# Kernel tuning notes

Hardware: AMD Instinct MI355X
Metric: run time of the kernel (lower is better)

## Reference

```python
import jax, jax.numpy as jnp
import numpy as np

B, S, D_MODEL, H = 2, 2048, 1024, 16
DEPTH = D_MODEL // H


def setup_inputs() -> dict:
    key = jax.random.key(0)
    ks = jax.random.split(key, 12)
    s = 1.0 / np.sqrt(D_MODEL)
    inp = {
        "q": jax.random.normal(ks[0], (B, S, D_MODEL), jnp.float32),
        "k": jax.random.normal(ks[1], (B, S, D_MODEL), jnp.float32),
        "v": jax.random.normal(ks[2], (B, S, D_MODEL), jnp.float32),
        # CTRL-style causal mask: 1 where position is disallowed (future), 0 otherwise
        "mask": jnp.triu(jnp.ones((S, S), jnp.float32), k=1),
        "Wq_w": jax.random.normal(ks[3], (D_MODEL, D_MODEL), jnp.float32) * s,
        "Wq_b": jax.random.normal(ks[4], (D_MODEL,), jnp.float32) * s,
        "Wk_w": jax.random.normal(ks[5], (D_MODEL, D_MODEL), jnp.float32) * s,
        "Wk_b": jax.random.normal(ks[6], (D_MODEL,), jnp.float32) * s,
        "Wv_w": jax.random.normal(ks[7], (D_MODEL, D_MODEL), jnp.float32) * s,
        "Wv_b": jax.random.normal(ks[8], (D_MODEL,), jnp.float32) * s,
        "dense_w": jax.random.normal(ks[9], (D_MODEL, D_MODEL), jnp.float32) * s,
        "dense_b": jax.random.normal(ks[10], (D_MODEL,), jnp.float32) * s,
    }
    return inp


def _split_heads(x):
    # [B, S, D] -> [B, H, S, depth]
    b, s, _ = x.shape
    return x.reshape(b, s, H, DEPTH).transpose(0, 2, 1, 3)


def reference(q, k, v, mask, Wq_w, Wq_b, Wk_w, Wk_b, Wv_w, Wv_b, dense_w, dense_b):
    b = q.shape[0]
    # torch Linear: y = x @ W^T + b
    qh = _split_heads(q @ Wq_w.T + Wq_b)  # [B,H,Sq,dh]
    kh = _split_heads(k @ Wk_w.T + Wk_b)  # [B,H,Sk,dh]
    vh = _split_heads(v @ Wv_w.T + Wv_b)  # [B,H,Sk,dh]

    scale = 1.0 / np.sqrt(DEPTH)
    logits = jnp.einsum("bhqd,bhkd->bhqk", qh, kh) * scale  # [B,H,Sq,Sk]
    nd, ns = logits.shape[-2], logits.shape[-1]
    logits = logits + mask[ns - nd:ns, :ns] * -10000.0
    attn = jax.nn.softmax(logits, axis=-1)
    ctx = jnp.einsum("bhqk,bhkd->bhqd", attn, vh)  # [B,H,Sq,dh]
    ctx = ctx.transpose(0, 2, 1, 3).reshape(b, -1, D_MODEL)  # [B,Sq,D]
    out = ctx @ dense_w.T + dense_b
    return out
```

## Files before the change

### kernel.cpp

```cpp
#include <hip/hip_runtime.h>
#include <hip/hip_bf16.h>

typedef __bf16 bf16x8 __attribute__((ext_vector_type(8)));
typedef __bf16 bf16x4 __attribute__((ext_vector_type(4)));
typedef float  f32x4  __attribute__((ext_vector_type(4)));

#define D_MODEL 1024
#define SEQ     2048
#define NH      16
#define DH      64
#define MTOT    4096

__device__ __forceinline__ void gload16(const void* gp, void* lp) {
  __builtin_amdgcn_global_load_lds(
      (const __attribute__((address_space(1))) unsigned int*)gp,
      (__attribute__((address_space(3))) unsigned int*)lp,
      16, 0, 0);
}

struct CvtSegs {
  const float* s[7];
  __bf16*      d[7];
  int          n8[7];
};

__global__ __launch_bounds__(256) void cvt_kernel(CvtSegs c) {
  const int seg = blockIdx.y;
  const float4* s = (const float4*)c.s[seg];
  bf16x8*       d = (bf16x8*)c.d[seg];
  const int n8 = c.n8[seg];
  for (int i = blockIdx.x * 256 + threadIdx.x; i < n8; i += gridDim.x * 256) {
    float4 a = s[2 * i];
    float4 b = s[2 * i + 1];
    bf16x8 o;
    o[0] = (__bf16)a.x; o[1] = (__bf16)a.y; o[2] = (__bf16)a.z; o[3] = (__bf16)a.w;
    o[4] = (__bf16)b.x; o[5] = (__bf16)b.y; o[6] = (__bf16)b.z; o[7] = (__bf16)b.w;
    d[i] = o;
  }
}

template <int EPI>
__device__ __forceinline__ void gemm_core(const __bf16* __restrict__ A,
                                          const __bf16* __restrict__ W,
                                          const float* __restrict__ bias,
                                          void* __restrict__ outp,
                                          __bf16* Asm, __bf16* Bsm,
                                          int row0, int col0) {
  const int tid = threadIdx.x;
  const int lane = tid & 63;
  const int w = tid >> 6;
  const int lr = lane & 15, lg = lane >> 4;
  const int wr = w >> 1, wc = w & 1;
  char* AsB = (char*)Asm;
  char* BsB = (char*)Bsm;

  f32x4 acc[4][4];
#pragma unroll
  for (int i = 0; i < 4; ++i)
#pragma unroll
    for (int j = 0; j < 4; ++j) acc[i][j] = (f32x4){0.f, 0.f, 0.f, 0.f};

  const int kch = (lane & 3) * 8;

#pragma unroll
  for (int tt = 0; tt < 2; ++tt) {
#pragma unroll
    for (int s = 0; s < 2; ++s) {
      const int cb = (w * 2 + s) * 64;
      const int arow = (cb + lane) >> 2;
      gload16(A + (size_t)(row0 + arow) * D_MODEL + tt * 32 + kch,
              AsB + tt * 8192 + cb * 16);
      gload16(W + (size_t)(col0 + arow) * D_MODEL + tt * 32 + kch,
              BsB + tt * 8192 + cb * 16);
    }
  }

  for (int t = 0; t < 32; ++t) {
    if (t < 31) asm volatile("s_waitcnt vmcnt(4)" ::: "memory");
    else        asm volatile("s_waitcnt vmcnt(0)" ::: "memory");
    __builtin_amdgcn_s_barrier();
    if (t + 2 < 32) {
      const int nb = (t + 2) % 3;
      const int k0 = (t + 2) * 32;
#pragma unroll
      for (int s = 0; s < 2; ++s) {
        const int cb = (w * 2 + s) * 64;
        const int arow = (cb + lane) >> 2;
        gload16(A + (size_t)(row0 + arow) * D_MODEL + k0 + kch,
                AsB + nb * 8192 + cb * 16);
        gload16(W + (size_t)(col0 + arow) * D_MODEL + k0 + kch,
                BsB + nb * 8192 + cb * 16);
      }
    }
    {
      char* Ab = AsB + (t % 3) * 8192;
      char* Bb = BsB + (t % 3) * 8192;
      bf16x8 af[4], bfr[4];
#pragma unroll
      for (int mi = 0; mi < 4; ++mi)
        af[mi] = *(const bf16x8*)(Ab + (wr * 64 + mi * 16 + lr) * 64 + lg * 16);
#pragma unroll
      for (int ni = 0; ni < 4; ++ni)
        bfr[ni] = *(const bf16x8*)(Bb + (wc * 64 + ni * 16 + lr) * 64 + lg * 16);
      __builtin_amdgcn_s_setprio(1);
#pragma unroll
      for (int mi = 0; mi < 4; ++mi)
#pragma unroll
        for (int ni = 0; ni < 4; ++ni)
          acc[mi][ni] = __builtin_amdgcn_mfma_f32_16x16x32_bf16(af[mi], bfr[ni],
                                                                acc[mi][ni], 0, 0, 0);
      __builtin_amdgcn_s_setprio(0);
      __builtin_amdgcn_sched_barrier(0);
    }
  }

  if (EPI == 2) {
    __bf16* o = (__bf16*)outp;
#pragma unroll
    for (int mi = 0; mi < 4; ++mi) {
#pragma unroll
      for (int ni = 0; ni < 4; ++ni) {
        const int n = col0 + wc * 64 + ni * 16 + lr;
        const float bv = bias[n];
        const int m0 = row0 + wr * 64 + mi * 16 + lg * 4;
        bf16x4 pk;
#pragma unroll
        for (int j = 0; j < 4; ++j) pk[j] = (__bf16)(acc[mi][ni][j] + bv);
        *(bf16x4*)(o + ((size_t)((m0 >> 11) * NH + (n >> 6)) * DH + (n & 63)) * SEQ +
                   (m0 & 2047)) = pk;
      }
    }
  } else {
#pragma unroll
    for (int mi = 0; mi < 4; ++mi) {
#pragma unroll
      for (int ni = 0; ni < 4; ++ni) {
        const int n = col0 + wc * 64 + ni * 16 + lr;
        const float bv = bias[n];
#pragma unroll
        for (int j = 0; j < 4; ++j) {
          const int m = row0 + wr * 64 + mi * 16 + lg * 4 + j;
          const float v = acc[mi][ni][j] + bv;
          if (EPI == 0) {
            __bf16* o = (__bf16*)outp;
            o[(size_t)((m >> 11) * NH + (n >> 6)) * (SEQ * DH) +
              (size_t)(m & 2047) * DH + (n & 63)] = (__bf16)v;
          } else {
            float* o = (float*)outp;
            o[(size_t)m * D_MODEL + n] = v;
          }
        }
      }
    }
  }
}

struct QkvPtrs {
  const __bf16* A[3];
  const __bf16* W[3];
  const float*  b[3];
  __bf16*       o[3];
};

__global__ __launch_bounds__(256, 3) void gemm_qkv_kernel(QkvPtrs p) {
  __shared__ __bf16 As[3][128 * 32];
  __shared__ __bf16 Bs[3][128 * 32];
  const int z = blockIdx.z;
  if (z == 2)
    gemm_core<2>(p.A[z], p.W[z], p.b[z], p.o[z], &As[0][0], &Bs[0][0],
                 blockIdx.x * 128, blockIdx.y * 128);
  else
    gemm_core<0>(p.A[z], p.W[z], p.b[z], p.o[z], &As[0][0], &Bs[0][0],
                 blockIdx.x * 128, blockIdx.y * 128);
}

__global__ __launch_bounds__(256, 3) void gemm_out_kernel(const __bf16* __restrict__ A,
                                                          const __bf16* __restrict__ W,
                                                          const float* __restrict__ b,
                                                          float* __restrict__ o) {
  __shared__ __bf16 As[3][128 * 32];
  __shared__ __bf16 Bs[3][128 * 32];
  gemm_core<1>(A, W, b, o, &As[0][0], &Bs[0][0], blockIdx.x * 128, blockIdx.y * 128);
}

__global__ __launch_bounds__(256, 2) void attn_kernel(const __bf16* __restrict__ qh,
                                                      const __bf16* __restrict__ kh,
                                                      const __bf16* __restrict__ vt,
                                                      __bf16* __restrict__ ctx) {
  __shared__ __align__(16) char LDS[81920];

  const int bh = blockIdx.x;
  const int qb = 31 - blockIdx.y;
  const int tid = threadIdx.x, lane = tid & 63, w = tid >> 6;
  const int lr = lane & 15, lg = lane >> 4;
  const size_t hoff = (size_t)bh * SEQ * DH;
  const __bf16* Q   = qh + hoff;
  const __bf16* Kp  = kh + hoff;
  const __bf16* Vtp = vt + hoff;
  const int q0 = qb * 64;

  bf16x8 qf[4][2];
#pragma unroll
  for (int qi = 0; qi < 4; ++qi)
#pragma unroll
    for (int ki = 0; ki < 2; ++ki)
      qf[qi][ki] = *(const bf16x8*)(Q + (size_t)(q0 + qi * 16 + lr) * DH +
                                    ki * 32 + lg * 8);

  f32x4 o[4][4];
#pragma unroll
  for (int qi = 0; qi < 4; ++qi)
#pragma unroll
    for (int ni = 0; ni < 4; ++ni) o[qi][ni] = (f32x4){0.f, 0.f, 0.f, 0.f};
  float ls[4] = {0.f, 0.f, 0.f, 0.f};

  char* Kl = LDS + w * 20480;
  char* Vl = Kl + 8192;
  char* Pl = Kl + 16384;

  const int ntt = 2 * qb + 2;
  const int cnt = (ntt - w + 3) >> 2;

#define STAGE_TILE(T, B)                                                      \
  {                                                                           \
    _Pragma("unroll") for (int g = 0; g < 4; ++g) {                           \
      const int c = g * 64 + lane;                                            \
      const int kr = c >> 3, kc2 = (c & 7) ^ (kr & 7);                        \
      gload16(Kp + (size_t)((T) * 32 + kr) * DH + kc2 * 8,                    \
              Kl + (B) * 4096 + g * 1024);                                    \
    }                                                                         \
    _Pragma("unroll") for (int g = 0; g < 4; ++g) {                           \
      const int c = g * 64 + lane;                                            \
      const int vr = c >> 2, vc2 = (c & 3) ^ (vr & 3);                        \
      gload16(Vtp + (size_t)vr * SEQ + (T) * 32 + vc2 * 8,                    \
              Vl + (B) * 4096 + g * 1024);                                    \
    }                                                                         \
  }

  if (cnt > 0) STAGE_TILE(w, 0);

  int cur = 0;
  for (int it = 0; it < cnt; ++it) {
    const int t = w + it * 4;
    if (it + 1 < cnt) {
      STAGE_TILE(t + 4, cur ^ 1);
      asm volatile("s_waitcnt vmcnt(8)" ::: "memory");
    } else {
      asm volatile("s_waitcnt vmcnt(0)" ::: "memory");
    }
    __builtin_amdgcn_sched_barrier(0);
    char* Kb = Kl + cur * 4096;
    char* Vb = Vl + cur * 4096;

    f32x4 st[2][4];
#pragma unroll
    for (int ni = 0; ni < 2; ++ni)
#pragma unroll
      for (int qi = 0; qi < 4; ++qi) st[ni][qi] = (f32x4){0.f, 0.f, 0.f, 0.f};
    __builtin_amdgcn_s_setprio(1);
#pragma unroll
    for (int ki = 0; ki < 2; ++ki) {
#pragma unroll
      for (int ni = 0; ni < 2; ++ni) {
        const int kr = ni * 16 + lr;
        bf16x8 kf = *(const bf16x8*)(Kb + kr * 128 +
                                     (((ki * 4 + lg) ^ (kr & 7)) << 4));
#pragma unroll
        for (int qi = 0; qi < 4; ++qi)
          st[ni][qi] = __builtin_amdgcn_mfma_f32_16x16x32_bf16(kf, qf[qi][ki],
                                                               st[ni][qi], 0, 0, 0);
      }
    }
    __builtin_amdgcn_s_setprio(0);

    const int kvb = t * 32;
    const bool needmask = (kvb + 31 > q0);
#pragma unroll
    for (int ni = 0; ni < 2; ++ni) {
#pragma unroll
      for (int qi = 0; qi < 4; ++qi) {
        bf16x4 pk;
#pragma unroll
        for (int j = 0; j < 4; ++j) {
          float v = st[ni][qi][j] * 0.18033688f;
          if (needmask && (kvb + ni * 16 + lg * 4 + j > q0 + qi * 16 + lr))
            v = -1e9f;
          const float pe = __builtin_amdgcn_exp2f(v);
          ls[qi] += pe;
          pk[j] = (__bf16)pe;
        }
        const int q = qi * 16 + lr;
        const int ch = (ni * 2 + (lg >> 1)) ^ (q & 3);
        *(bf16x4*)(Pl + q * 64 + ch * 16 + (lg & 1) * 8) = pk;
      }
    }
    asm volatile("s_waitcnt lgkmcnt(0)" ::: "memory");
    __builtin_amdgcn_sched_barrier(0);

    bf16x8 pf[4], vf[4];
#pragma unroll
    for (int qi = 0; qi < 4; ++qi) {
      const int q = qi * 16 + lr;
      pf[qi] = *(const bf16x8*)(Pl + q * 64 + ((lg ^ (q & 3)) << 4));
    }
#pragma unroll
    for (int ni = 0; ni < 4; ++ni) {
      const int d = ni * 16 + lr;
      vf[ni] = *(const bf16x8*)(Vb + d * 64 + ((lg ^ (d & 3)) << 4));
    }
    __builtin_amdgcn_s_setprio(1);
#pragma unroll
    for (int qi = 0; qi < 4; ++qi)
#pragma unroll
      for (int ni = 0; ni < 4; ++ni)
        o[qi][ni] = __builtin_amdgcn_mfma_f32_16x16x32_bf16(pf[qi], vf[ni],
                                                            o[qi][ni], 0, 0, 0);
    __builtin_amdgcn_s_setprio(0);
    cur ^= 1;
  }
#undef STAGE_TILE

  __syncthreads();
  float* Op = (float*)LDS + w * 4352;
#pragma unroll
  for (int qi = 0; qi < 4; ++qi)
#pragma unroll
    for (int ni = 0; ni < 4; ++ni)
      *(f32x4*)(Op + (ni * 16 + lr) * 68 + qi * 16 + lg * 4) = o[qi][ni];
  {
    float* Lp = (float*)LDS + 17408 + (w * 4 + lg) * 64;
#pragma unroll
    for (int qi = 0; qi < 4; ++qi) Lp[qi * 16 + lr] = ls[qi];
  }
  __syncthreads();

  f32x4 a2[4];
#pragma unroll
  for (int r = 0; r < 4; ++r) a2[r] = (f32x4){0.f, 0.f, 0.f, 0.f};
#pragma unroll
  for (int p = 0; p < 4; ++p) {
    const float* Pp = (const float*)LDS + p * 4352;
#pragma unroll
    for (int r = 0; r < 4; ++r)
      a2[r] += *(const f32x4*)(Pp + (r * 16 + lr) * 68 + w * 16 + lg * 4);
  }
  float Lt = 0.f;
#pragma unroll
  for (int k = 0; k < 4; ++k)
    Lt += ((const float*)LDS)[17408 + (k * 4 + lg) * 64 + w * 16 + lr];
  Lt += __shfl_xor(Lt, 16, 64);
  Lt += __shfl_xor(Lt, 32, 64);

  const int bb = bh >> 4, hh = bh & 15;
#pragma unroll
  for (int j = 0; j < 4; ++j) {
    const float inv = 1.0f / __shfl(Lt, lg * 4 + j, 16);
    const int qrow = q0 + w * 16 + lg * 4 + j;
    __bf16* orow = ctx + (size_t)(bb * SEQ + qrow) * D_MODEL + hh * DH;
#pragma unroll
    for (int r = 0; r < 4; ++r)
      orow[r * 16 + lr] = (__bf16)(a2[r][j] * inv);
  }
}

extern "C" void kernel_launch(void* const* d_in, const int* in_sizes, int n_in,
                              void* d_out, int out_size, void* d_ws, size_t ws_size,
                              hipStream_t stream) {
  (void)in_sizes; (void)n_in; (void)out_size; (void)ws_size;
  const float* q  = (const float*)d_in[0];
  const float* k  = (const float*)d_in[1];
  const float* v  = (const float*)d_in[2];
  const float* Wq = (const float*)d_in[4];
  const float* bq = (const float*)d_in[5];
  const float* Wk = (const float*)d_in[6];
  const float* bk = (const float*)d_in[7];
  const float* Wv = (const float*)d_in[8];
  const float* bv = (const float*)d_in[9];
  const float* Wd = (const float*)d_in[10];
  const float* bd = (const float*)d_in[11];

  char* ws = (char*)d_ws;
  __bf16* qb  = (__bf16*)(ws + 0);
  __bf16* kb  = (__bf16*)(ws + 8388608);
  __bf16* vb  = (__bf16*)(ws + 16777216);
  __bf16* wqb = (__bf16*)(ws + 25165824);
  __bf16* wkb = (__bf16*)(ws + 27262976);
  __bf16* wvb = (__bf16*)(ws + 29360128);
  __bf16* wdb = (__bf16*)(ws + 31457280);
  __bf16* qhp = (__bf16*)(ws + 33554432);
  __bf16* khp = (__bf16*)(ws + 41943040);
  __bf16* vtp = (__bf16*)(ws + 50331648);
  __bf16* ctxp= (__bf16*)(ws + 58720256);

  CvtSegs cs;
  cs.s[0] = q;  cs.d[0] = qb;  cs.n8[0] = 524288;
  cs.s[1] = k;  cs.d[1] = kb;  cs.n8[1] = 524288;
  cs.s[2] = v;  cs.d[2] = vb;  cs.n8[2] = 524288;
  cs.s[3] = Wq; cs.d[3] = wqb; cs.n8[3] = 131072;
  cs.s[4] = Wk; cs.d[4] = wkb; cs.n8[4] = 131072;
  cs.s[5] = Wv; cs.d[5] = wvb; cs.n8[5] = 131072;
  cs.s[6] = Wd; cs.d[6] = wdb; cs.n8[6] = 131072;
  cvt_kernel<<<dim3(256, 7, 1), dim3(256), 0, stream>>>(cs);

  QkvPtrs qp;
  qp.A[0] = qb;  qp.A[1] = kb;  qp.A[2] = vb;
  qp.W[0] = wqb; qp.W[1] = wkb; qp.W[2] = wvb;
  qp.b[0] = bq;  qp.b[1] = bk;  qp.b[2] = bv;
  qp.o[0] = qhp; qp.o[1] = khp; qp.o[2] = vtp;
  gemm_qkv_kernel<<<dim3(32, 8, 3), dim3(256), 0, stream>>>(qp);

  attn_kernel<<<dim3(32, 32, 1), dim3(256), 0, stream>>>(qhp, khp, vtp, ctxp);

  gemm_out_kernel<<<dim3(32, 8, 1), dim3(256), 0, stream>>>(ctxp, wdb, bd, (float*)d_out);
}
```

Baseline: 114.9 us.

## Use 256x256 tiles with 512-thread blocks for the QKV projection GEMM

The fused QKV projection moves from 128x128 tiles with 256 threads to 256x256 tiles with 512 threads (8 waves, each computing 128x64), keeping triple-buffered LDS staging via global_load_lds. Larger tiles double the arithmetic done per loaded element and cut global/L2 traffic for the A and W operands. The grid shrinks from 768 to 192 blocks, which can underfill a 256-CU device and leave tail imbalance, and the larger accumulator arrays raise register pressure. The output GEMM is split into its own f32-epilogue core and is otherwise unchanged.

Result: slower. 128.6 us (+11.9%).

```diff
diff --git a/kernel.cpp b/kernel.cpp
--- a/kernel.cpp
+++ b/kernel.cpp
@@ -40,12 +40,131 @@
 }
 
 template <int EPI>
-__device__ __forceinline__ void gemm_core(const __bf16* __restrict__ A,
-                                          const __bf16* __restrict__ W,
-                                          const float* __restrict__ bias,
-                                          void* __restrict__ outp,
-                                          __bf16* Asm, __bf16* Bsm,
-                                          int row0, int col0) {
+__device__ __forceinline__ void gemm256_core(const __bf16* __restrict__ A,
+                                             const __bf16* __restrict__ W,
+                                             const float* __restrict__ bias,
+                                             void* __restrict__ outp,
+                                             __bf16* Asm, __bf16* Bsm,
+                                             int row0, int col0) {
+  const int tid = threadIdx.x;
+  const int lane = tid & 63;
+  const int w = tid >> 6;
+  const int lr = lane & 15, lg = lane >> 4;
+  const int wr = w >> 2, wc = w & 3;
+  char* AsB = (char*)Asm;
+  char* BsB = (char*)Bsm;
+
+  f32x4 acc[8][4];
+#pragma unroll
+  for (int i = 0; i < 8; ++i)
+#pragma unroll
+    for (int j = 0; j < 4; ++j) acc[i][j] = (f32x4){0.f, 0.f, 0.f, 0.f};
+
+#define STAGE256(TT, B)                                                       \
+  {                                                                           \
+    _Pragma("unroll") for (int s = 0; s < 2; ++s) {                           \
+      const int cb = (s * 8 + w) * 64;                                        \
+      const int c = cb + lane;                                                \
+      const int row = c >> 2;                                                 \
+      const int kch = (c & 3) * 8;                                            \
+      gload16(A + (size_t)(row0 + row) * D_MODEL + (TT) * 32 + kch,           \
+              AsB + (B) * 16384 + cb * 16);                                   \
+      gload16(W + (size_t)(col0 + row) * D_MODEL + (TT) * 32 + kch,           \
+              BsB + (B) * 16384 + cb * 16);                                   \
+    }                                                                         \
+  }
+
+  STAGE256(0, 0);
+  STAGE256(1, 1);
+
+  for (int t = 0; t < 32; ++t) {
+    if (t < 31) asm volatile("s_waitcnt vmcnt(4)" ::: "memory");
+    else        asm volatile("s_waitcnt vmcnt(0)" ::: "memory");
+    __builtin_amdgcn_s_barrier();
+    if (t + 2 < 32) STAGE256(t + 2, (t + 2) % 3);
+    {
+      char* Ab = AsB + (t % 3) * 16384;
+      char* Bb = BsB + (t % 3) * 16384;
+      bf16x8 af[8], bfr[4];
+#pragma unroll
+      for (int mi = 0; mi < 8; ++mi)
+        af[mi] = *(const bf16x8*)(Ab + (wr * 128 + mi * 16 + lr) * 64 + lg * 16);
+#pragma unroll
+      for (int ni = 0; ni < 4; ++ni)
+        bfr[ni] = *(const bf16x8*)(Bb + (wc * 64 + ni * 16 + lr) * 64 + lg * 16);
+      __builtin_amdgcn_s_setprio(1);
+#pragma unroll
+      for (int mi = 0; mi < 8; ++mi)
+#pragma unroll
+        for (int ni = 0; ni < 4; ++ni)
+          acc[mi][ni] = __builtin_amdgcn_mfma_f32_16x16x32_bf16(af[mi], bfr[ni],
+                                                                acc[mi][ni], 0, 0, 0);
+      __builtin_amdgcn_s_setprio(0);
+      __builtin_amdgcn_sched_barrier(0);
+    }
+  }
+#undef STAGE256
+
+  if (EPI == 2) {
+    __bf16* o = (__bf16*)outp;
+#pragma unroll
+    for (int mi = 0; mi < 8; ++mi) {
+#pragma unroll
+      for (int ni = 0; ni < 4; ++ni) {
+        const int n = col0 + wc * 64 + ni * 16 + lr;
+        const float bv = bias[n];
+        const int m0 = row0 + wr * 128 + mi * 16 + lg * 4;
+        bf16x4 pk;
+#pragma unroll
+        for (int j = 0; j < 4; ++j) pk[j] = (__bf16)(acc[mi][ni][j] + bv);
+        *(bf16x4*)(o + ((size_t)((m0 >> 11) * NH + (n >> 6)) * DH + (n & 63)) * SEQ +
+                   (m0 & 2047)) = pk;
+      }
+    }
+  } else {
+#pragma unroll
+    for (int mi = 0; mi < 8; ++mi) {
+#pragma unroll
+      for (int ni = 0; ni < 4; ++ni) {
+        const int n = col0 + wc * 64 + ni * 16 + lr;
+        const float bv = bias[n];
+#pragma unroll
+        for (int j = 0; j < 4; ++j) {
+          const int m = row0 + wr * 128 + mi * 16 + lg * 4 + j;
+          __bf16* o = (__bf16*)outp;
+          o[(size_t)((m >> 11) * NH + (n >> 6)) * (SEQ * DH) +
+            (size_t)(m & 2047) * DH + (n & 63)] = (__bf16)(acc[mi][ni][j] + bv);
+        }
+      }
+    }
+  }
+}
+
+struct QkvPtrs {
+  const __bf16* A[3];
+  const __bf16* W[3];
+  const float*  b[3];
+  __bf16*       o[3];
+};
+
+__global__ __launch_bounds__(512, 2) void gemm_qkv_kernel(QkvPtrs p) {
+  __shared__ __bf16 As[3][256 * 32];
+  __shared__ __bf16 Bs[3][256 * 32];
+  const int z = blockIdx.z;
+  if (z == 2)
+    gemm256_core<2>(p.A[z], p.W[z], p.b[z], p.o[z], &As[0][0], &Bs[0][0],
+                    blockIdx.x * 256, blockIdx.y * 256);
+  else
+    gemm256_core<0>(p.A[z], p.W[z], p.b[z], p.o[z], &As[0][0], &Bs[0][0],
+                    blockIdx.x * 256, blockIdx.y * 256);
+}
+
+__device__ __forceinline__ void gemm_core_f32(const __bf16* __restrict__ A,
+                                              const __bf16* __restrict__ W,
+                                              const float* __restrict__ bias,
+                                              float* __restrict__ outp,
+                                              __bf16* Asm, __bf16* Bsm,
+                                              int row0, int col0) {
   const int tid = threadIdx.x;
   const int lane = tid & 63;
   const int w = tid >> 6;
@@ -114,64 +233,19 @@
     }
   }
 
-  if (EPI == 2) {
-    __bf16* o = (__bf16*)outp;
-#pragma unroll
-    for (int mi = 0; mi < 4; ++mi) {
-#pragma unroll
-      for (int ni = 0; ni < 4; ++ni) {
-        const int n = col0 + wc * 64 + ni * 16 + lr;
-        const float bv = bias[n];
-        const int m0 = row0 + wr * 64 + mi * 16 + lg * 4;
-        bf16x4 pk;
-#pragma unroll
-        for (int j = 0; j < 4; ++j) pk[j] = (__bf16)(acc[mi][ni][j] + bv);
-        *(bf16x4*)(o + ((size_t)((m0 >> 11) * NH + (n >> 6)) * DH + (n & 63)) * SEQ +
-                   (m0 & 2047)) = pk;
-      }
-    }
-  } else {
-#pragma unroll
-    for (int mi = 0; mi < 4; ++mi) {
-#pragma unroll
-      for (int ni = 0; ni < 4; ++ni) {
-        const int n = col0 + wc * 64 + ni * 16 + lr;
-        const float bv = bias[n];
-#pragma unroll
-        for (int j = 0; j < 4; ++j) {
-          const int m = row0 + wr * 64 + mi * 16 + lg * 4 + j;
-          const float v = acc[mi][ni][j] + bv;
-          if (EPI == 0) {
-            __bf16* o = (__bf16*)outp;
-            o[(size_t)((m >> 11) * NH + (n >> 6)) * (SEQ * DH) +
-              (size_t)(m & 2047) * DH + (n & 63)] = (__bf16)v;
-          } else {
-            float* o = (float*)outp;
-            o[(size_t)m * D_MODEL + n] = v;
-          }
-        }
-      }
-    }
-  }
-}
-
-struct QkvPtrs {
-  const __bf16* A[3];
-  const __bf16* W[3];
-  const float*  b[3];
-  __bf16*       o[3];
-};
-
-__global__ __launch_bounds__(256, 3) void gemm_qkv_kernel(QkvPtrs p) {
-  __shared__ __bf16 As[3][128 * 32];
-  __shared__ __bf16 Bs[3][128 * 32];
-  const int z = blockIdx.z;
-  if (z == 2)
-    gemm_core<2>(p.A[z], p.W[z], p.b[z], p.o[z], &As[0][0], &Bs[0][0],
-                 blockIdx.x * 128, blockIdx.y * 128);
-  else
-    gemm_core<0>(p.A[z], p.W[z], p.b[z], p.o[z], &As[0][0], &Bs[0][0],
-                 blockIdx.x * 128, blockIdx.y * 128);
+#pragma unroll
+  for (int mi = 0; mi < 4; ++mi) {
+#pragma unroll
+    for (int ni = 0; ni < 4; ++ni) {
+      const int n = col0 + wc * 64 + ni * 16 + lr;
+      const float bv = bias[n];
+#pragma unroll
+      for (int j = 0; j < 4; ++j) {
+        const int m = row0 + wr * 64 + mi * 16 + lg * 4 + j;
+        outp[(size_t)m * D_MODEL + n] = acc[mi][ni][j] + bv;
+      }
+    }
+  }
 }
 
 __global__ __launch_bounds__(256, 3) void gemm_out_kernel(const __bf16* __restrict__ A,
@@ -180,7 +254,7 @@
                                                           float* __restrict__ o) {
   __shared__ __bf16 As[3][128 * 32];
   __shared__ __bf16 Bs[3][128 * 32];
-  gemm_core<1>(A, W, b, o, &As[0][0], &Bs[0][0], blockIdx.x * 128, blockIdx.y * 128);
+  gemm_core_f32(A, W, b, o, &As[0][0], &Bs[0][0], blockIdx.x * 128, blockIdx.y * 128);
 }
 
 __global__ __launch_bounds__(256, 2) void attn_kernel(const __bf16* __restrict__ qh,
@@ -407,7 +481,7 @@
   qp.W[0] = wqb; qp.W[1] = wkb; qp.W[2] = wvb;
   qp.b[0] = bq;  qp.b[1] = bk;  qp.b[2] = bv;
   qp.o[0] = qhp; qp.o[1] = khp; qp.o[2] = vtp;
-  gemm_qkv_kernel<<<dim3(32, 8, 3), dim3(256), 0, stream>>>(qp);
+  gemm_qkv_kernel<<<dim3(16, 4, 3), dim3(512), 0, stream>>>(qp);
 
   attn_kernel<<<dim3(32, 32, 1), dim3(256), 0, stream>>>(qhp, khp, vtp, ctxp);
 
```

## Shrink attention KV tile to 16 and keep P in registers via k16 MFMA

Applied to the files above, without the earlier changes.

The attention kernel now processes 16-key tiles per wave instead of 32, so the exponentiated scores stay in registers and feed a 16x16x16 bf16 MFMA directly as the B operand, with no round trip through LDS for P. LDS per block drops by half, so launch bounds move from 2 to 3 blocks per CU for higher occupancy. The cross-wave reduction now stores partial outputs as bf16 in a transposed layout. In exchange the loop runs twice as many iterations with smaller MFMAs, and the bf16 partial sums lose some precision.

Result: faster. 112.6 us (-2.0%).

```diff
diff --git a/kernel.cpp b/kernel.cpp
--- a/kernel.cpp
+++ b/kernel.cpp
@@ -4,12 +4,21 @@
 typedef __bf16 bf16x8 __attribute__((ext_vector_type(8)));
 typedef __bf16 bf16x4 __attribute__((ext_vector_type(4)));
 typedef float  f32x4  __attribute__((ext_vector_type(4)));
+typedef short  s16x4  __attribute__((ext_vector_type(4)));
 
 #define D_MODEL 1024
 #define SEQ     2048
 #define NH      16
 #define DH      64
 #define MTOT    4096
+
+__device__ __forceinline__ f32x4 mfma_bf16_k16(s16x4 a, s16x4 b, f32x4 c) {
+#if defined(__HIP_DEVICE_COMPILE__)
+  return __builtin_amdgcn_mfma_f32_16x16x16bf16_1k(a, b, c, 0, 0, 0);
+#else
+  return c;
+#endif
+}
 
 __device__ __forceinline__ void gload16(const void* gp, void* lp) {
   __builtin_amdgcn_global_load_lds(
@@ -183,11 +192,11 @@
   gemm_core<1>(A, W, b, o, &As[0][0], &Bs[0][0], blockIdx.x * 128, blockIdx.y * 128);
 }
 
-__global__ __launch_bounds__(256, 2) void attn_kernel(const __bf16* __restrict__ qh,
+__global__ __launch_bounds__(256, 3) void attn_kernel(const __bf16* __restrict__ qh,
                                                       const __bf16* __restrict__ kh,
                                                       const __bf16* __restrict__ vt,
                                                       __bf16* __restrict__ ctx) {
-  __shared__ __align__(16) char LDS[81920];
+  __shared__ __align__(16) char LDS[40960];
 
   const int bh = blockIdx.x;
   const int qb = 31 - blockIdx.y;
@@ -207,128 +216,115 @@
       qf[qi][ki] = *(const bf16x8*)(Q + (size_t)(q0 + qi * 16 + lr) * DH +
                                     ki * 32 + lg * 8);
 
-  f32x4 o[4][4];
-#pragma unroll
-  for (int qi = 0; qi < 4; ++qi)
-#pragma unroll
-    for (int ni = 0; ni < 4; ++ni) o[qi][ni] = (f32x4){0.f, 0.f, 0.f, 0.f};
+  f32x4 o2[4][4];
+#pragma unroll
+  for (int ni = 0; ni < 4; ++ni)
+#pragma unroll
+    for (int qi = 0; qi < 4; ++qi) o2[ni][qi] = (f32x4){0.f, 0.f, 0.f, 0.f};
   float ls[4] = {0.f, 0.f, 0.f, 0.f};
 
-  char* Kl = LDS + w * 20480;
-  char* Vl = Kl + 8192;
-  char* Pl = Kl + 16384;
-
-  const int ntt = 2 * qb + 2;
-  const int cnt = (ntt - w + 3) >> 2;
+  char* Kl = LDS + w * 8192;
+  char* Vl = Kl + 4096;
+
+  const int cnt = qb + 1;
 
 #define STAGE_TILE(T, B)                                                      \
   {                                                                           \
-    _Pragma("unroll") for (int g = 0; g < 4; ++g) {                           \
+    _Pragma("unroll") for (int g = 0; g < 2; ++g) {                           \
       const int c = g * 64 + lane;                                            \
-      const int kr = c >> 3, kc2 = (c & 7) ^ (kr & 7);                        \
-      gload16(Kp + (size_t)((T) * 32 + kr) * DH + kc2 * 8,                    \
-              Kl + (B) * 4096 + g * 1024);                                    \
+      const int kr = c >> 3, gch = (c & 7) ^ (kr & 7);                        \
+      gload16(Kp + (size_t)((T) * 16 + kr) * DH + gch * 8,                    \
+              Kl + (B) * 2048 + g * 1024);                                    \
     }                                                                         \
-    _Pragma("unroll") for (int g = 0; g < 4; ++g) {                           \
+    _Pragma("unroll") for (int g = 0; g < 2; ++g) {                           \
       const int c = g * 64 + lane;                                            \
-      const int vr = c >> 2, vc2 = (c & 3) ^ (vr & 3);                        \
-      gload16(Vtp + (size_t)vr * SEQ + (T) * 32 + vc2 * 8,                    \
-              Vl + (B) * 4096 + g * 1024);                                    \
+      const int vd = c >> 1, gvh = (c & 1) ^ ((vd >> 2) & 1);                 \
+      gload16(Vtp + (size_t)vd * SEQ + (T) * 16 + gvh * 8,                    \
+              Vl + (B) * 2048 + g * 1024);                                    \
     }                                                                         \
   }
 
-  if (cnt > 0) STAGE_TILE(w, 0);
+  STAGE_TILE(w, 0);
 
   int cur = 0;
   for (int it = 0; it < cnt; ++it) {
     const int t = w + it * 4;
     if (it + 1 < cnt) {
       STAGE_TILE(t + 4, cur ^ 1);
-      asm volatile("s_waitcnt vmcnt(8)" ::: "memory");
+      asm volatile("s_waitcnt vmcnt(4)" ::: "memory");
     } else {
       asm volatile("s_waitcnt vmcnt(0)" ::: "memory");
     }
     __builtin_amdgcn_sched_barrier(0);
-    char* Kb = Kl + cur * 4096;
-    char* Vb = Vl + cur * 4096;
-
-    f32x4 st[2][4];
-#pragma unroll
-    for (int ni = 0; ni < 2; ++ni)
-#pragma unroll
-      for (int qi = 0; qi < 4; ++qi) st[ni][qi] = (f32x4){0.f, 0.f, 0.f, 0.f};
+    char* Kb = Kl + cur * 2048;
+    char* Vb = Vl + cur * 2048;
+
+    f32x4 st[4];
+#pragma unroll
+    for (int qi = 0; qi < 4; ++qi) st[qi] = (f32x4){0.f, 0.f, 0.f, 0.f};
     __builtin_amdgcn_s_setprio(1);
 #pragma unroll
     for (int ki = 0; ki < 2; ++ki) {
-#pragma unroll
-      for (int ni = 0; ni < 2; ++ni) {
-        const int kr = ni * 16 + lr;
-        bf16x8 kf = *(const bf16x8*)(Kb + kr * 128 +
-                                     (((ki * 4 + lg) ^ (kr & 7)) << 4));
-#pragma unroll
-        for (int qi = 0; qi < 4; ++qi)
-          st[ni][qi] = __builtin_amdgcn_mfma_f32_16x16x32_bf16(kf, qf[qi][ki],
-                                                               st[ni][qi], 0, 0, 0);
-      }
+      bf16x8 kf = *(const bf16x8*)(Kb + lr * 128 +
+                                   (((ki * 4 + lg) ^ (lr & 7)) << 4));
+#pragma unroll
+      for (int qi = 0; qi < 4; ++qi)
+        st[qi] = __builtin_amdgcn_mfma_f32_16x16x32_bf16(kf, qf[qi][ki],
+                                                         st[qi], 0, 0, 0);
     }
     __builtin_amdgcn_s_setprio(0);
 
-    const int kvb = t * 32;
-    const bool needmask = (kvb + 31 > q0);
-#pragma unroll
-    for (int ni = 0; ni < 2; ++ni) {
-#pragma unroll
-      for (int qi = 0; qi < 4; ++qi) {
-        bf16x4 pk;
-#pragma unroll
-        for (int j = 0; j < 4; ++j) {
-          float v = st[ni][qi][j] * 0.18033688f;
-          if (needmask && (kvb + ni * 16 + lg * 4 + j > q0 + qi * 16 + lr))
-            v = -1e9f;
-          const float pe = __builtin_amdgcn_exp2f(v);
-          ls[qi] += pe;
-          pk[j] = (__bf16)pe;
-        }
-        const int q = qi * 16 + lr;
-        const int ch = (ni * 2 + (lg >> 1)) ^ (q & 3);
-        *(bf16x4*)(Pl + q * 64 + ch * 16 + (lg & 1) * 8) = pk;
-      }
-    }
-    asm volatile("s_waitcnt lgkmcnt(0)" ::: "memory");
-    __builtin_amdgcn_sched_barrier(0);
-
-    bf16x8 pf[4], vf[4];
+    const int kvb = t * 16;
+    const bool needmask = (kvb + 15 > q0);
+    bf16x4 pk[4];
 #pragma unroll
     for (int qi = 0; qi < 4; ++qi) {
-      const int q = qi * 16 + lr;
-      pf[qi] = *(const bf16x8*)(Pl + q * 64 + ((lg ^ (q & 3)) << 4));
-    }
+#pragma unroll
+      for (int j = 0; j < 4; ++j) {
+        float v = st[qi][j] * 0.18033688f;
+        if (needmask && (kvb + lg * 4 + j > q0 + qi * 16 + lr)) v = -1e9f;
+        const float pe = __builtin_amdgcn_exp2f(v);
+        ls[qi] += pe;
+        pk[qi][j] = (__bf16)pe;
+      }
+    }
+
+    bf16x4 vf[4];
 #pragma unroll
     for (int ni = 0; ni < 4; ++ni) {
       const int d = ni * 16 + lr;
-      vf[ni] = *(const bf16x8*)(Vb + d * 64 + ((lg ^ (d & 3)) << 4));
+      vf[ni] = *(const bf16x4*)(Vb + d * 32 +
+                                ((((lg >> 1) ^ ((d >> 2) & 1)) << 4)) + (lg & 1) * 8);
     }
     __builtin_amdgcn_s_setprio(1);
 #pragma unroll
-    for (int qi = 0; qi < 4; ++qi)
-#pragma unroll
-      for (int ni = 0; ni < 4; ++ni)
-        o[qi][ni] = __builtin_amdgcn_mfma_f32_16x16x32_bf16(pf[qi], vf[ni],
-                                                            o[qi][ni], 0, 0, 0);
+    for (int ni = 0; ni < 4; ++ni) {
+      const s16x4 va = *(const s16x4*)&vf[ni];
+#pragma unroll
+      for (int qi = 0; qi < 4; ++qi) {
+        const s16x4 pb = *(const s16x4*)&pk[qi];
+        o2[ni][qi] = mfma_bf16_k16(va, pb, o2[ni][qi]);
+      }
+    }
     __builtin_amdgcn_s_setprio(0);
     cur ^= 1;
   }
 #undef STAGE_TILE
 
   __syncthreads();
-  float* Op = (float*)LDS + w * 4352;
-#pragma unroll
-  for (int qi = 0; qi < 4; ++qi)
-#pragma unroll
-    for (int ni = 0; ni < 4; ++ni)
-      *(f32x4*)(Op + (ni * 16 + lr) * 68 + qi * 16 + lg * 4) = o[qi][ni];
   {
-    float* Lp = (float*)LDS + 17408 + (w * 4 + lg) * 64;
+    char* Ow = LDS + w * 8704;
+#pragma unroll
+    for (int qi = 0; qi < 4; ++qi) {
+#pragma unroll
+      for (int ni = 0; ni < 4; ++ni) {
+        bf16x4 pkk;
+#pragma unroll
+        for (int j = 0; j < 4; ++j) pkk[j] = (__bf16)o2[ni][qi][j];
+        *(bf16x4*)(Ow + (qi * 16 + lr) * 136 + (ni * 16 + lg * 4) * 2) = pkk;
+      }
+    }
+    float* Lp = (float*)(LDS + 34816) + w * 256 + lg * 64;
 #pragma unroll
     for (int qi = 0; qi < 4; ++qi) Lp[qi * 16 + lr] = ls[qi];
   }
@@ -339,17 +335,18 @@
   for (int r = 0; r < 4; ++r) a2[r] = (f32x4){0.f, 0.f, 0.f, 0.f};
 #pragma unroll
   for (int p = 0; p < 4; ++p) {
-    const float* Pp = (const float*)LDS + p * 4352;
+    const char* Pp = LDS + p * 8704;
 #pragma unroll
     for (int r = 0; r < 4; ++r)
-      a2[r] += *(const f32x4*)(Pp + (r * 16 + lr) * 68 + w * 16 + lg * 4);
+#pragma unroll
+      for (int j = 0; j < 4; ++j)
+        a2[r][j] += (float)*(const __bf16*)(Pp + (w * 16 + lg * 4 + j) * 136 +
+                                            (r * 16 + lr) * 2);
   }
   float Lt = 0.f;
 #pragma unroll
-  for (int k = 0; k < 4; ++k)
-    Lt += ((const float*)LDS)[17408 + (k * 4 + lg) * 64 + w * 16 + lr];
-  Lt += __shfl_xor(Lt, 16, 64);
-  Lt += __shfl_xor(Lt, 32, 64);
+  for (int k = 0; k < 16; ++k)
+    Lt += ((const float*)(LDS + 34816))[k * 64 + w * 16 + lr];
 
   const int bb = bh >> 4, hh = bh & 15;
 #pragma unroll
```
